# Kernel optimization log

Hardware: AMD Instinct MI355X
Metric: run time of the kernel (lower is better)

The kernel has to match this reference:

```python
import jax, jax.numpy as jnp
import numpy as np

N_NODES = 150000
D = 64
N_EDGES = 2000000  # bidirectional: 2 * num_train_edges


def setup_inputs() -> dict:
    key = jax.random.key(0)
    k1, k2, k3, k4, k5 = jax.random.split(key, 5)
    nodes_emb = jax.random.normal(k1, (N_NODES, D), dtype=jnp.float32)
    src = jax.random.randint(k2, (N_EDGES,), 0, N_NODES, dtype=jnp.int64 if jax.config.jax_enable_x64 else jnp.int32).astype(jnp.int32)
    dst = jax.random.randint(k3, (N_EDGES,), 0, N_NODES, dtype=jnp.int32)
    W1 = jax.random.normal(k4, (2 * D, D), dtype=jnp.float32) * (1.0 / np.sqrt(2 * D))
    b1 = jnp.zeros((D,), dtype=jnp.float32)
    W2 = jax.random.normal(k5, (D, 1), dtype=jnp.float32) * (1.0 / np.sqrt(D))
    b2 = jnp.zeros((1,), dtype=jnp.float32)
    return {"nodes_emb": nodes_emb, "src": src, "dst": dst,
            "W1": W1, "b1": b1, "W2": W2, "b2": b2}


def reference(nodes_emb, src, dst, W1, b1, W2, b2):
    # Gather per-edge endpoint embeddings and concat: [E, 2D]
    emb_src = nodes_emb[src]          # [E, D]
    emb_dst = nodes_emb[dst]          # [E, D]
    edge_emb = jnp.concatenate([emb_src, emb_dst], axis=1)  # [E, 2D]
    # 2-layer MLP edge scorer: Linear(2D->D) -> ReLU -> Linear(D->1)
    h = jax.nn.relu(edge_emb @ W1 + b1)  # [E, D]
    edge_logits = h @ W2 + b2            # [E, 1]
    return edge_logits
```

## Files before the change

### kernel.cpp

```cpp
#include <hip/hip_runtime.h>

typedef __attribute__((ext_vector_type(8))) short bf16x8;
typedef __attribute__((ext_vector_type(4))) float f32x4;
typedef __attribute__((ext_vector_type(2))) unsigned int u32x2;
typedef __attribute__((ext_vector_type(4))) unsigned int u32x4;

#define LDSTR 136
#define TPW 8

static __device__ __forceinline__ unsigned int pack2bf(float x, float y) {
  unsigned int ux = __builtin_bit_cast(unsigned int, x);
  ux += 0x7fffu + ((ux >> 16) & 1u);
  unsigned int uy = __builtin_bit_cast(unsigned int, y);
  uy += 0x7fffu + ((uy >> 16) & 1u);
  return (ux >> 16) | (uy & 0xffff0000u);
}
static __device__ __forceinline__ unsigned short f2bf_s(float x) {
  unsigned int ux = __builtin_bit_cast(unsigned int, x);
  ux += 0x7fffu + ((ux >> 16) & 1u);
  return (unsigned short)(ux >> 16);
}
static __device__ __forceinline__ bf16x8 make_afrag(float4 lo, float4 hi) {
  u32x4 p;
  p[0] = pack2bf(lo.x, lo.y);
  p[1] = pack2bf(lo.z, lo.w);
  p[2] = pack2bf(hi.x, hi.y);
  p[3] = pack2bf(hi.z, hi.w);
  return __builtin_bit_cast(bf16x8, p);
}

__global__ __launch_bounds__(256) void node_proj(
    const float* __restrict__ emb,
    const float* __restrict__ W1,
    const float* __restrict__ b1,
    u32x2* __restrict__ P,
    u32x2* __restrict__ Q,
    int N, int ntiles)
{
  __shared__ unsigned short ls_w1t[64 * LDSTR];
  const int tid  = threadIdx.x;
  const int wave = tid >> 6;
  const int lane = tid & 63;
  const int l15  = lane & 15;
  const int quad = lane >> 4;

  for (int i = tid; i < 64 * 128; i += 256) {
    int k = i >> 6, n = i & 63;
    ls_w1t[n * LDSTR + k] = f2bf_s(W1[i]);
  }
  __syncthreads();

  float b1q[4];
  #pragma unroll
  for (int tn = 0; tn < 4; ++tn) b1q[tn] = b1[tn * 16 + l15];

  bf16x8 bfragP[4][2], bfragQ[4][2];
  #pragma unroll
  for (int tn = 0; tn < 4; ++tn)
    #pragma unroll
    for (int s = 0; s < 2; ++s) {
      bfragP[tn][s] = *(const bf16x8*)&ls_w1t[(tn * 16 + l15) * LDSTR + s * 32 + quad * 8];
      bfragQ[tn][s] = *(const bf16x8*)&ls_w1t[(tn * 16 + l15) * LDSTR + 64 + s * 32 + quad * 8];
    }

  for (int tile = blockIdx.x * 4 + wave; tile < ntiles; tile += gridDim.x * 4) {
    const int base = tile * 16;

    bf16x8 afr0, afr1;
    {
      int node = base + l15;
      node = (node < N) ? node : N - 1;
      const float* rp = emb + (long long)node * 64 + quad * 8;
      afr0 = make_afrag(*(const float4*)(rp),      *(const float4*)(rp + 4));
      afr1 = make_afrag(*(const float4*)(rp + 32), *(const float4*)(rp + 36));
    }

    f32x4 aP[4], aQ[4];
    #pragma unroll
    for (int tn = 0; tn < 4; ++tn) { aP[tn] = (f32x4){0,0,0,0}; aQ[tn] = (f32x4){0,0,0,0}; }
    #pragma unroll
    for (int tn = 0; tn < 4; ++tn) {
      aP[tn] = __builtin_amdgcn_mfma_f32_16x16x32_bf16(afr0, bfragP[tn][0], aP[tn], 0, 0, 0);
      aQ[tn] = __builtin_amdgcn_mfma_f32_16x16x32_bf16(afr0, bfragQ[tn][0], aQ[tn], 0, 0, 0);
      aP[tn] = __builtin_amdgcn_mfma_f32_16x16x32_bf16(afr1, bfragP[tn][1], aP[tn], 0, 0, 0);
      aQ[tn] = __builtin_amdgcn_mfma_f32_16x16x32_bf16(afr1, bfragQ[tn][1], aQ[tn], 0, 0, 0);
    }

    #pragma unroll
    for (int r = 0; r < 4; ++r) {
      const int m = base + quad * 4 + r;
      if (m < N) {
        u32x2 vp, vq;
        vp[0] = pack2bf(aP[0][r], aP[1][r]);
        vp[1] = pack2bf(aP[2][r], aP[3][r]);
        vq[0] = pack2bf(aQ[0][r] + b1q[0], aQ[1][r] + b1q[1]);
        vq[1] = pack2bf(aQ[2][r] + b1q[2], aQ[3][r] + b1q[3]);
        P[(long long)m * 16 + l15] = vp;
        Q[(long long)m * 16 + l15] = vq;
      }
    }
  }
}

__global__ __launch_bounds__(256) void edge_score(
    const unsigned short* __restrict__ P,
    const unsigned short* __restrict__ Q,
    const int*   __restrict__ src,
    const int*   __restrict__ dst,
    const float* __restrict__ W2,
    const float* __restrict__ b2,
    float*       __restrict__ out,
    int E)
{
  const int tid  = blockIdx.x * 256 + threadIdx.x;
  const int lane = threadIdx.x & 63;
  const int s    = lane & 7;
  const int g    = lane >> 3;
  const int wid  = tid >> 6;
  const int step = gridDim.x * 4 * 32;

  float w2v[8];
  #pragma unroll
  for (int j = 0; j < 8; ++j) {
    const int pos = s * 8 + j;
    const int ch  = (pos & 3) * 16 + (pos >> 2);
    w2v[j] = W2[ch];
  }
  const float b2v = b2[0];
  const int so = s * 8;

#define DOT8(PV, QV, ACC)                                                     \
  {                                                                           \
    u32x4 pu = __builtin_bit_cast(u32x4, PV);                                 \
    u32x4 qu = __builtin_bit_cast(u32x4, QV);                                 \
    _Pragma("unroll")                                                         \
    for (int i = 0; i < 4; ++i) {                                             \
      float pl = __builtin_bit_cast(float, pu[i] << 16);                      \
      float ph = __builtin_bit_cast(float, pu[i] & 0xffff0000u);              \
      float ql = __builtin_bit_cast(float, qu[i] << 16);                      \
      float qh = __builtin_bit_cast(float, qu[i] & 0xffff0000u);              \
      float h0 = fmaxf(pl + ql, 0.f);                                         \
      float h1 = fmaxf(ph + qh, 0.f);                                         \
      ACC = __builtin_fmaf(h0, w2v[2 * i], ACC);                              \
      ACC = __builtin_fmaf(h1, w2v[2 * i + 1], ACC);                          \
    }                                                                         \
  }

  int e0 = wid * 32;
  if (e0 >= E) return;

  int iA, iB, iC, iD, jA, jB, jC, jD;
  {
    const int eA = e0 + g,      eAc = (eA < E) ? eA : E - 1;
    const int eB = e0 + 8 + g,  eBc = (eB < E) ? eB : E - 1;
    const int eC = e0 + 16 + g, eCc = (eC < E) ? eC : E - 1;
    const int eD = e0 + 24 + g, eDc = (eD < E) ? eD : E - 1;
    iA = src[eAc]; jA = dst[eAc];
    iB = src[eBc]; jB = dst[eBc];
    iC = src[eCc]; jC = dst[eCc];
    iD = src[eDc]; jD = dst[eDc];
  }

  while (true) {
    const bf16x8 pA = *(const bf16x8*)(P + iA * 64 + so);
    const bf16x8 qA = *(const bf16x8*)(Q + jA * 64 + so);
    const bf16x8 pB = *(const bf16x8*)(P + iB * 64 + so);
    const bf16x8 qB = *(const bf16x8*)(Q + jB * 64 + so);
    const bf16x8 pC = *(const bf16x8*)(P + iC * 64 + so);
    const bf16x8 qC = *(const bf16x8*)(Q + jC * 64 + so);
    const bf16x8 pD = *(const bf16x8*)(P + iD * 64 + so);
    const bf16x8 qD = *(const bf16x8*)(Q + jD * 64 + so);

    const int en = e0 + step;
    const bool more = (en < E);
    if (more) {
      const int fA = en + g,      fAc = (fA < E) ? fA : E - 1;
      const int fB = en + 8 + g,  fBc = (fB < E) ? fB : E - 1;
      const int fC = en + 16 + g, fCc = (fC < E) ? fC : E - 1;
      const int fD = en + 24 + g, fDc = (fD < E) ? fD : E - 1;
      iA = src[fAc]; jA = dst[fAc];
      iB = src[fBc]; jB = dst[fBc];
      iC = src[fCc]; jC = dst[fCc];
      iD = src[fDc]; jD = dst[fDc];
    }

    float accA = 0.f, accB = 0.f, accC = 0.f, accD = 0.f;
    DOT8(pA, qA, accA);
    DOT8(pB, qB, accB);
    DOT8(pC, qC, accC);
    DOT8(pD, qD, accD);

    accA += __shfl_xor(accA, 1); accB += __shfl_xor(accB, 1);
    accC += __shfl_xor(accC, 1); accD += __shfl_xor(accD, 1);
    accA += __shfl_xor(accA, 2); accB += __shfl_xor(accB, 2);
    accC += __shfl_xor(accC, 2); accD += __shfl_xor(accD, 2);
    accA += __shfl_xor(accA, 4); accB += __shfl_xor(accB, 4);
    accC += __shfl_xor(accC, 4); accD += __shfl_xor(accD, 4);

    if (s == 0) {
      const int eA = e0 + g;
      const int eB = e0 + 8 + g;
      const int eC = e0 + 16 + g;
      const int eD = e0 + 24 + g;
      if (eA < E) out[eA] = accA + b2v;
      if (eB < E) out[eB] = accB + b2v;
      if (eC < E) out[eC] = accC + b2v;
      if (eD < E) out[eD] = accD + b2v;
    }

    if (!more) break;
    e0 = en;
  }
#undef DOT8
}

__global__ __launch_bounds__(256) void edge_mlp_f32(
    const float* __restrict__ nodes_emb, const int* __restrict__ src,
    const int* __restrict__ dst, const float* __restrict__ W1,
    const float* __restrict__ b1, const float* __restrict__ W2,
    const float* __restrict__ b2, float* __restrict__ out, int E)
{
  __shared__ unsigned short ls_w1t[64 * LDSTR];
  __shared__ float ls_b1[64];
  __shared__ float ls_w2[64];
  const int tid = threadIdx.x, wave = tid >> 6, lane = tid & 63;
  const int l15 = lane & 15, quad = lane >> 4;
  for (int i = tid; i < 64 * 128; i += 256) {
    int n = i >> 7, k = i & 127;
    ls_w1t[n * LDSTR + k] = f2bf_s(W1[k * 64 + n]);
  }
  if (tid < 64) { ls_b1[tid] = b1[tid]; ls_w2[tid] = W2[tid]; }
  __syncthreads();
  bf16x8 bfrag[4][4];
  #pragma unroll
  for (int tn = 0; tn < 4; ++tn)
    #pragma unroll
    for (int s = 0; s < 4; ++s)
      bfrag[tn][s] = *(const bf16x8*)&ls_w1t[(tn * 16 + l15) * LDSTR + s * 32 + quad * 8];
  float myb1[4], myw2[4];
  #pragma unroll
  for (int tn = 0; tn < 4; ++tn) { myb1[tn] = ls_b1[tn*16+l15]; myw2[tn] = ls_w2[tn*16+l15]; }
  const float b2v = b2[0];
  const int wave_base = blockIdx.x * (TPW * 64) + wave * (TPW * 16);
  #pragma unroll 1
  for (int t = 0; t < TPW; ++t) {
    const int tile_base = wave_base + t * 16;
    if (tile_base >= E) break;
    const int e = tile_base + l15;
    const int si = src[e], di = dst[e];
    const float* srow = nodes_emb + (long long)si * 64 + quad * 8;
    const float* drow = nodes_emb + (long long)di * 64 + quad * 8;
    float4 v0 = *(const float4*)(srow),      v1 = *(const float4*)(srow + 4);
    float4 v2 = *(const float4*)(srow + 32), v3 = *(const float4*)(srow + 36);
    float4 v4 = *(const float4*)(drow),      v5 = *(const float4*)(drow + 4);
    float4 v6 = *(const float4*)(drow + 32), v7 = *(const float4*)(drow + 36);
    bf16x8 afr[4] = {make_afrag(v0,v1), make_afrag(v2,v3), make_afrag(v4,v5), make_afrag(v6,v7)};
    f32x4 acc[4];
    #pragma unroll
    for (int tn = 0; tn < 4; ++tn) acc[tn] = (f32x4){0.f,0.f,0.f,0.f};
    #pragma unroll
    for (int s = 0; s < 4; ++s)
      #pragma unroll
      for (int tn = 0; tn < 4; ++tn)
        acc[tn] = __builtin_amdgcn_mfma_f32_16x16x32_bf16(afr[s], bfrag[tn][s], acc[tn], 0, 0, 0);
    #pragma unroll
    for (int r = 0; r < 4; ++r) {
      float p = 0.f;
      #pragma unroll
      for (int tn = 0; tn < 4; ++tn) {
        float h = fmaxf(acc[tn][r] + myb1[tn], 0.f);
        p = __builtin_fmaf(h, myw2[tn], p);
      }
      p += __shfl_xor(p, 1); p += __shfl_xor(p, 2);
      p += __shfl_xor(p, 4); p += __shfl_xor(p, 8);
      if (l15 == 0) out[tile_base + quad * 4 + r] = p + b2v;
    }
  }
}

extern "C" void kernel_launch(void* const* d_in, const int* in_sizes, int n_in,
                              void* d_out, int out_size, void* d_ws, size_t ws_size,
                              hipStream_t stream) {
  const float* nodes_emb = (const float*)d_in[0];
  const int*   src       = (const int*)d_in[1];
  const int*   dst       = (const int*)d_in[2];
  const float* W1        = (const float*)d_in[3];
  const float* b1        = (const float*)d_in[4];
  const float* W2        = (const float*)d_in[5];
  const float* b2        = (const float*)d_in[6];
  float* out = (float*)d_out;

  const int E = in_sizes[1];
  const int nodes_elems = in_sizes[0];
  const int N = nodes_elems / 64;
  const size_t szP = (size_t)nodes_elems * 2;
  const size_t need = szP * 2;

  if (ws_size >= need) {
    u32x2* P = (u32x2*)d_ws;
    u32x2* Q = (u32x2*)((char*)d_ws + szP);
    const int ntiles = (N + 15) / 16;
    hipLaunchKernelGGL(node_proj, dim3(512), dim3(256), 0, stream,
                       nodes_emb, W1, b1, P, Q, N, ntiles);
    hipLaunchKernelGGL(edge_score, dim3(2048), dim3(256), 0, stream,
                       (const unsigned short*)P, (const unsigned short*)Q,
                       src, dst, W2, b2, out, E);
  } else {
    const int epb = TPW * 64;
    const int blocks = (E + epb - 1) / epb;
    hipLaunchKernelGGL(edge_mlp_f32, dim3(blocks), dim3(256), 0, stream,
                       nodes_emb, src, dst, W1, b1, W2, b2, out, E);
  }
}
```

Measured before the change: 172.6 us.

## Quantize per-node projections to int8 with per-row scales for edge gather

The node projection kernel now stores P and Q as 8-bit values offset by 128, with one float scale per row taken from the row's max absolute value (found by a wave shuffle reduction), instead of bf16. The edge kernel gathers half as many bytes per endpoint plus one scale per endpoint, then dequantizes with FMAs before the ReLU and the W2 dot product. The aim is to halve the bandwidth of the random gathers, which dominate the edge pass. The costs are extra scale loads, more ALU work per element, and quantization error that could break accuracy tolerance. The edge grid is also doubled.

```diff
diff --git a/kernel.cpp b/kernel.cpp
--- a/kernel.cpp
+++ b/kernel.cpp
@@ -29,12 +29,18 @@
   return __builtin_bit_cast(bf16x8, p);
 }
 
+static __device__ __forceinline__ unsigned int q8(float v, float inv) {
+  return (unsigned int)((int)rintf(v * inv) + 128);
+}
+
 __global__ __launch_bounds__(256) void node_proj(
     const float* __restrict__ emb,
     const float* __restrict__ W1,
     const float* __restrict__ b1,
-    u32x2* __restrict__ P,
-    u32x2* __restrict__ Q,
+    unsigned int* __restrict__ P8,
+    unsigned int* __restrict__ Q8,
+    float* __restrict__ SP,
+    float* __restrict__ SQ,
     int N, int ntiles)
 {
   __shared__ unsigned short ls_w1t[64 * LDSTR];
@@ -89,22 +95,41 @@
     #pragma unroll
     for (int r = 0; r < 4; ++r) {
       const int m = base + quad * 4 + r;
+      float vp0 = aP[0][r], vp1 = aP[1][r], vp2 = aP[2][r], vp3 = aP[3][r];
+      float vq0 = aQ[0][r] + b1q[0], vq1 = aQ[1][r] + b1q[1];
+      float vq2 = aQ[2][r] + b1q[2], vq3 = aQ[3][r] + b1q[3];
+
+      float mp = fmaxf(fmaxf(fabsf(vp0), fabsf(vp1)), fmaxf(fabsf(vp2), fabsf(vp3)));
+      float mq = fmaxf(fmaxf(fabsf(vq0), fabsf(vq1)), fmaxf(fabsf(vq2), fabsf(vq3)));
+      mp = fmaxf(mp, __shfl_xor(mp, 1)); mq = fmaxf(mq, __shfl_xor(mq, 1));
+      mp = fmaxf(mp, __shfl_xor(mp, 2)); mq = fmaxf(mq, __shfl_xor(mq, 2));
+      mp = fmaxf(mp, __shfl_xor(mp, 4)); mq = fmaxf(mq, __shfl_xor(mq, 4));
+      mp = fmaxf(mp, __shfl_xor(mp, 8)); mq = fmaxf(mq, __shfl_xor(mq, 8));
+
+      const float invP = (mp > 0.f) ? 127.f / mp : 0.f;
+      const float invQ = (mq > 0.f) ? 127.f / mq : 0.f;
+
       if (m < N) {
-        u32x2 vp, vq;
-        vp[0] = pack2bf(aP[0][r], aP[1][r]);
-        vp[1] = pack2bf(aP[2][r], aP[3][r]);
-        vq[0] = pack2bf(aQ[0][r] + b1q[0], aQ[1][r] + b1q[1]);
-        vq[1] = pack2bf(aQ[2][r] + b1q[2], aQ[3][r] + b1q[3]);
-        P[(long long)m * 16 + l15] = vp;
-        Q[(long long)m * 16 + l15] = vq;
+        unsigned int pw = q8(vp0, invP) | (q8(vp1, invP) << 8) |
+                          (q8(vp2, invP) << 16) | (q8(vp3, invP) << 24);
+        unsigned int qw = q8(vq0, invQ) | (q8(vq1, invQ) << 8) |
+                          (q8(vq2, invQ) << 16) | (q8(vq3, invQ) << 24);
+        P8[(long long)m * 16 + l15] = pw;
+        Q8[(long long)m * 16 + l15] = qw;
+        if (l15 == 0) {
+          SP[m] = mp * (1.f / 127.f);
+          SQ[m] = mq * (1.f / 127.f);
+        }
       }
     }
   }
 }
 
 __global__ __launch_bounds__(256) void edge_score(
-    const unsigned short* __restrict__ P,
-    const unsigned short* __restrict__ Q,
+    const unsigned int* __restrict__ P8,
+    const unsigned int* __restrict__ Q8,
+    const float* __restrict__ SP,
+    const float* __restrict__ SQ,
     const int*   __restrict__ src,
     const int*   __restrict__ dst,
     const float* __restrict__ W2,
@@ -127,22 +152,22 @@
     w2v[j] = W2[ch];
   }
   const float b2v = b2[0];
-  const int so = s * 8;
-
-#define DOT8(PV, QV, ACC)                                                     \
+  const int sd = s * 2;
+
+#define DOT8I(PU, QU, SPv, SQv, ACC)                                          \
   {                                                                           \
-    u32x4 pu = __builtin_bit_cast(u32x4, PV);                                 \
-    u32x4 qu = __builtin_bit_cast(u32x4, QV);                                 \
+    const float t_ = __builtin_fmaf(-128.f, SPv + SQv, 0.f);                  \
     _Pragma("unroll")                                                         \
-    for (int i = 0; i < 4; ++i) {                                             \
-      float pl = __builtin_bit_cast(float, pu[i] << 16);                      \
-      float ph = __builtin_bit_cast(float, pu[i] & 0xffff0000u);              \
-      float ql = __builtin_bit_cast(float, qu[i] << 16);                      \
-      float qh = __builtin_bit_cast(float, qu[i] & 0xffff0000u);              \
-      float h0 = fmaxf(pl + ql, 0.f);                                         \
-      float h1 = fmaxf(ph + qh, 0.f);                                         \
-      ACC = __builtin_fmaf(h0, w2v[2 * i], ACC);                              \
-      ACC = __builtin_fmaf(h1, w2v[2 * i + 1], ACC);                          \
+    for (int k = 0; k < 2; ++k) {                                             \
+      const unsigned int pd = PU[k], qd = QU[k];                              \
+      _Pragma("unroll")                                                       \
+      for (int b = 0; b < 4; ++b) {                                           \
+        float pf = (float)((pd >> (8 * b)) & 0xffu);                          \
+        float qf = (float)((qd >> (8 * b)) & 0xffu);                          \
+        float h = __builtin_fmaf(pf, SPv, __builtin_fmaf(qf, SQv, t_));       \
+        h = fmaxf(h, 0.f);                                                    \
+        ACC = __builtin_fmaf(h, w2v[k * 4 + b], ACC);                         \
+      }                                                                       \
     }                                                                         \
   }
 
@@ -160,35 +185,41 @@
     iC = src[eCc]; jC = dst[eCc];
     iD = src[eDc]; jD = dst[eDc];
   }
+  float spA = SP[iA], sqA = SQ[jA];
+  float spB = SP[iB], sqB = SQ[jB];
+  float spC = SP[iC], sqC = SQ[jC];
+  float spD = SP[iD], sqD = SQ[jD];
 
   while (true) {
-    const bf16x8 pA = *(const bf16x8*)(P + iA * 64 + so);
-    const bf16x8 qA = *(const bf16x8*)(Q + jA * 64 + so);
-    const bf16x8 pB = *(const bf16x8*)(P + iB * 64 + so);
-    const bf16x8 qB = *(const bf16x8*)(Q + jB * 64 + so);
-    const bf16x8 pC = *(const bf16x8*)(P + iC * 64 + so);
-    const bf16x8 qC = *(const bf16x8*)(Q + jC * 64 + so);
-    const bf16x8 pD = *(const bf16x8*)(P + iD * 64 + so);
-    const bf16x8 qD = *(const bf16x8*)(Q + jD * 64 + so);
+    const u32x2 pA = *(const u32x2*)(P8 + iA * 16 + sd);
+    const u32x2 qA = *(const u32x2*)(Q8 + jA * 16 + sd);
+    const u32x2 pB = *(const u32x2*)(P8 + iB * 16 + sd);
+    const u32x2 qB = *(const u32x2*)(Q8 + jB * 16 + sd);
+    const u32x2 pC = *(const u32x2*)(P8 + iC * 16 + sd);
+    const u32x2 qC = *(const u32x2*)(Q8 + jC * 16 + sd);
+    const u32x2 pD = *(const u32x2*)(P8 + iD * 16 + sd);
+    const u32x2 qD = *(const u32x2*)(Q8 + jD * 16 + sd);
 
     const int en = e0 + step;
     const bool more = (en < E);
+    int nA = iA, nB = iB, nC = iC, nD = iD;
+    int mA = jA, mB = jB, mC = jC, mD = jD;
     if (more) {
       const int fA = en + g,      fAc = (fA < E) ? fA : E - 1;
       const int fB = en + 8 + g,  fBc = (fB < E) ? fB : E - 1;
       const int fC = en + 16 + g, fCc = (fC < E) ? fC : E - 1;
       const int fD = en + 24 + g, fDc = (fD < E) ? fD : E - 1;
-      iA = src[fAc]; jA = dst[fAc];
-      iB = src[fBc]; jB = dst[fBc];
-      iC = src[fCc]; jC = dst[fCc];
-      iD = src[fDc]; jD = dst[fDc];
+      nA = src[fAc]; mA = dst[fAc];
+      nB = src[fBc]; mB = dst[fBc];
+      nC = src[fCc]; mC = dst[fCc];
+      nD = src[fDc]; mD = dst[fDc];
     }
 
     float accA = 0.f, accB = 0.f, accC = 0.f, accD = 0.f;
-    DOT8(pA, qA, accA);
-    DOT8(pB, qB, accB);
-    DOT8(pC, qC, accC);
-    DOT8(pD, qD, accD);
+    DOT8I(pA, qA, spA, sqA, accA);
+    DOT8I(pB, qB, spB, sqB, accB);
+    DOT8I(pC, qC, spC, sqC, accC);
+    DOT8I(pD, qD, spD, sqD, accD);
 
     accA += __shfl_xor(accA, 1); accB += __shfl_xor(accB, 1);
     accC += __shfl_xor(accC, 1); accD += __shfl_xor(accD, 1);
@@ -209,9 +240,15 @@
     }
 
     if (!more) break;
+    iA = nA; iB = nB; iC = nC; iD = nD;
+    jA = mA; jB = mB; jC = mC; jD = mD;
+    spA = SP[iA]; sqA = SQ[jA];
+    spB = SP[iB]; sqB = SQ[jB];
+    spC = SP[iC]; sqC = SQ[jC];
+    spD = SP[iD]; sqD = SQ[jD];
     e0 = en;
   }
-#undef DOT8
+#undef DOT8I
 }
 
 __global__ __launch_bounds__(256) void edge_mlp_f32(
@@ -293,18 +330,19 @@
   const int E = in_sizes[1];
   const int nodes_elems = in_sizes[0];
   const int N = nodes_elems / 64;
-  const size_t szP = (size_t)nodes_elems * 2;
-  const size_t need = szP * 2;
+  const size_t szRow = (size_t)N * 64;
+  const size_t need  = szRow * 2 + (size_t)N * 8;
 
   if (ws_size >= need) {
-    u32x2* P = (u32x2*)d_ws;
-    u32x2* Q = (u32x2*)((char*)d_ws + szP);
+    unsigned int* P8 = (unsigned int*)d_ws;
+    unsigned int* Q8 = (unsigned int*)((char*)d_ws + szRow);
+    float* SP = (float*)((char*)d_ws + szRow * 2);
+    float* SQ = (float*)((char*)d_ws + szRow * 2 + (size_t)N * 4);
     const int ntiles = (N + 15) / 16;
     hipLaunchKernelGGL(node_proj, dim3(512), dim3(256), 0, stream,
-                       nodes_emb, W1, b1, P, Q, N, ntiles);
-    hipLaunchKernelGGL(edge_score, dim3(2048), dim3(256), 0, stream,
-                       (const unsigned short*)P, (const unsigned short*)Q,
-                       src, dst, W2, b2, out, E);
+                       nodes_emb, W1, b1, P8, Q8, SP, SQ, N, ntiles);
+    hipLaunchKernelGGL(edge_score, dim3(4096), dim3(256), 0, stream,
+                       P8, Q8, SP, SQ, src, dst, W2, b2, out, E);
   } else {
     const int epb = TPW * 64;
     const int blocks = (E + epb - 1) / epb;
```

After: 175.9 us. Within noise of the previous version (+1.9%).
